# Performance work log

Measured on AMD Instinct MI355X. Metric: run time of the kernel, lower is better.

Reference implementation:

```python
import jax, jax.numpy as jnp
import numpy as np

EMBED_DIM = 128
NUM_SYMBOLS = 200000
PAD_IDX = NUM_SYMBOLS
PROCESS_STEPS = 4
LN_EPS = 1e-5
NEG_INF = -1.0e9


def _layernorm(x, g, b):
    m = jnp.mean(x, axis=-1, keepdims=True)
    v = jnp.var(x, axis=-1, keepdims=True)
    return (x - m) / jnp.sqrt(v + LN_EPS) * g + b


def setup_inputs() -> dict:
    key = jax.random.key(0)
    ks = jax.random.split(key, 32)
    d = EMBED_DIM
    B, FEW, K = 4096, 5, 50

    def n(i, shape, s=0.05):
        return jax.random.normal(ks[i], shape, dtype=jnp.float32) * s

    inp = {}
    inp["query"] = jax.random.randint(ks[0], (B, 2), 0, NUM_SYMBOLS)
    inp["support"] = jax.random.randint(ks[1], (FEW, 2), 0, NUM_SYMBOLS)
    inp["q_l1"] = jax.random.randint(ks[2], (B, K, 2), 0, NUM_SYMBOLS + 1)
    inp["q_deg_l"] = jax.random.randint(ks[3], (B,), 0, K + 1)
    inp["q_r1"] = jax.random.randint(ks[4], (B, K, 2), 0, NUM_SYMBOLS + 1)
    inp["q_deg_r"] = jax.random.randint(ks[5], (B,), 0, K + 1)
    inp["s_l1"] = jax.random.randint(ks[6], (FEW, K, 2), 0, NUM_SYMBOLS + 1)
    inp["s_deg_l"] = jax.random.randint(ks[7], (FEW,), 0, K + 1)
    inp["s_r1"] = jax.random.randint(ks[8], (FEW, K, 2), 0, NUM_SYMBOLS + 1)
    inp["s_deg_r"] = jax.random.randint(ks[9], (FEW,), 0, K + 1)
    # Embedding table with zeroed padding row (nn.Embedding padding_idx semantics)
    inp["emb"] = n(10, (NUM_SYMBOLS + 1, d), 0.1).at[PAD_IDX].set(0.0)
    inp["gcn_W"] = n(11, (d, 2 * d))
    inp["gcn_lin_b"] = jnp.zeros((d,), jnp.float32)
    inp["gcn_b"] = jnp.zeros((d,), jnp.float32)
    inp["gate_temp"] = jnp.float32(1.0)
    inp["cg_W1"] = n(12, (d // 2, d))
    inp["cg_b1"] = jnp.zeros((d // 2,), jnp.float32)
    inp["cg_ln_g"] = jnp.ones((d // 2,), jnp.float32)
    inp["cg_ln_b"] = jnp.zeros((d // 2,), jnp.float32)
    inp["cg_W2"] = n(13, (1, d // 2))
    inp["cg_b2"] = jnp.zeros((1,), jnp.float32)
    dm = 2 * d  # d_model
    inp["se_W1"] = n(14, (2 * dm, dm))
    inp["se_b1"] = jnp.zeros((2 * dm,), jnp.float32)
    inp["se_W2"] = n(15, (dm, 2 * dm))
    inp["se_b2"] = jnp.zeros((dm,), jnp.float32)
    inp["se_ln_g"] = jnp.ones((dm,), jnp.float32)
    inp["se_ln_b"] = jnp.zeros((dm,), jnp.float32)
    hid = 2 * dm  # LSTMCell hidden size
    inp["lstm_Wih"] = n(16, (4 * hid, dm))
    inp["lstm_Whh"] = n(17, (4 * hid, hid))
    inp["lstm_bih"] = jnp.zeros((4 * hid,), jnp.float32)
    inp["lstm_bhh"] = jnp.zeros((4 * hid,), jnp.float32)
    return inp


def reference(query, support, q_l1, q_deg_l, q_r1, q_deg_r, s_l1, s_deg_l, s_r1, s_deg_r,
              emb, gcn_W, gcn_lin_b, gcn_b, gate_temp,
              cg_W1, cg_b1, cg_ln_g, cg_ln_b, cg_W2, cg_b2,
              se_W1, se_b1, se_W2, se_b2, se_ln_g, se_ln_b,
              lstm_Wih, lstm_Whh, lstm_bih, lstm_bhh):

    def neigh(conns, deg, self_ids):
        rel, ent = conns[..., 0], conns[..., 1]
        self_e = emb[self_ids]                                      # [N, d]
        cat = jnp.concatenate([emb[rel], emb[ent]], axis=-1)        # [N, K, 2d]
        proj = jnp.einsum('nkc,dc->nkd', cat, gcn_W) + gcn_lin_b + gcn_b
        proj = jax.nn.leaky_relu(proj, 0.01)                        # dropout = eval no-op
        scores = jnp.einsum('nkd,nd->nk', proj, self_e)
        scores = jnp.where(rel == PAD_IDX, NEG_INF, scores)
        w = jax.nn.softmax(scores, axis=1)
        agg = jnp.einsum('nk,nkd->nd', w, proj)                     # [N, d]
        h = jax.nn.relu(_layernorm(agg @ cg_W1.T + cg_b1, cg_ln_g, cg_ln_b))
        logit = h @ cg_W2.T + cg_b2                                 # [N, 1]
        temp = jnp.clip(gate_temp, 0.1, 5.0)
        gate = jax.nn.sigmoid(logit / temp)
        gate = gate * (deg > 0).astype(jnp.float32)[:, None]
        return jnp.tanh(self_e + gate * agg)

    def support_enc(x):  # residual FFN + LayerNorm
        h = jax.nn.relu(x @ se_W1.T + se_b1)
        return _layernorm(h @ se_W2.T + se_b2 + x, se_ln_g, se_ln_b)

    q_vec = jnp.concatenate([neigh(q_l1, q_deg_l, query[:, 0]),
                             neigh(q_r1, q_deg_r, query[:, 1])], axis=-1)   # [B, 2d]
    s_vec = jnp.concatenate([neigh(s_l1, s_deg_l, support[:, 0]),
                             neigh(s_r1, s_deg_r, support[:, 1])], axis=-1)  # [FEW, 2d]

    support_g = jnp.mean(support_enc(s_vec), axis=0, keepdims=True)  # [1, 2d]
    query_enc = support_enc(q_vec)                                   # [B, 2d]

    B, dm = query_enc.shape
    hid = 2 * dm

    def step(carry, _):
        h_r, c = carry
        gates = query_enc @ lstm_Wih.T + lstm_bih + h_r @ lstm_Whh.T + lstm_bhh
        i, f, g, o = jnp.split(gates, 4, axis=-1)  # torch LSTMCell gate order
        c = jax.nn.sigmoid(f) * c + jax.nn.sigmoid(i) * jnp.tanh(g)
        h_cell = jax.nn.sigmoid(o) * jnp.tanh(c)
        h = query_enc + h_cell[:, :dm]
        attn = jax.nn.softmax(h @ support_g.T, axis=1)  # [B, 1]
        r = attn @ support_g
        return (jnp.concatenate([h, r], axis=1), c), h

    init = (jnp.zeros((B, hid), query_enc.dtype), jnp.zeros((B, hid), query_enc.dtype))
    _, hs = jax.lax.scan(step, init, None, length=PROCESS_STEPS)
    query_g = hs[-1]
    return jnp.sum(query_g * support_g, axis=1)  # [B]
```

## Files before the change

### kernel.cpp

```cpp
#include <hip/hip_runtime.h>
#include <hip/hip_bf16.h>
#include <cstdint>
#include <cstddef>

#define PAD_IDX 200000
#define KN 50
#define MROWS 200001

using frag8 = __attribute__((ext_vector_type(8))) short;
using f32x4 = __attribute__((ext_vector_type(4))) float;

__device__ __forceinline__ short f2bf_rn(float v) {
    __hip_bfloat16 h = __float2bfloat16(v);
    union { __hip_bfloat16 h; short s; } u; u.h = h; return u.s;
}
__device__ __forceinline__ float bf2f(short s) {
    union { uint32_t u; float f; } x; x.u = ((uint32_t)(uint16_t)s) << 16;
    return x.f;
}
__device__ __forceinline__ float sigm(float x) { return 1.f / (1.f + __expf(-x)); }

__device__ __forceinline__ int lstm_perm(int c) {
    int u = c >> 6, g = (c >> 4) & 3, v = c & 15;
    return (g << 9) + (u << 4) + v;
}

__global__ void k_prep(const float* __restrict__ se_W1, const float* __restrict__ se_W2,
                       const float* __restrict__ gcn_W, const float* __restrict__ lin_b,
                       const float* __restrict__ gb,
                       const float* __restrict__ Wih, const float* __restrict__ Whh,
                       short* __restrict__ sw1, short* __restrict__ sw2,
                       short* __restrict__ Bmat, float* __restrict__ bias256,
                       short* __restrict__ Bih, short* __restrict__ Bhh) {
    int b = blockIdx.x, t = threadIdx.x;
    if (b < 512) {
        int i = b * 256 + t;
        sw1[i] = f2bf_rn(se_W1[i]);
    } else if (b < 1024) {
        int i = (b - 512) * 256 + t;
        sw2[i] = f2bf_rn(se_W2[i]);
    } else if (b < 1152) {
        int i = (b - 1024) * 256 + t;
        int n = i >> 7, k = i & 127;
        float v = (n < 128) ? gcn_W[n * 256 + k] : gcn_W[(n - 128) * 256 + 128 + k];
        Bmat[i] = f2bf_rn(v);
        if (k == 0) bias256[n] = (n < 128) ? 0.f : (lin_b[n - 128] + gb[n - 128]);
    } else {
        int i = (b - 1152) * 256 + t;
        int c = i >> 9, k = i & 511;
        int n = lstm_perm(c);
        if (k < 256) Bih[c * 256 + k] = f2bf_rn(Wih[n * 256 + k]);
        else         Bhh[c * 256 + (k - 256)] = f2bf_rn(Whh[(size_t)n * 512 + (k - 256)]);
    }
}


__global__ __launch_bounds__(256, 2) void k_table(
    const float* __restrict__ emb, const short* __restrict__ Bmat,
    const float* __restrict__ bias256, short* __restrict__ T)
{
    __shared__ short Bs[128 * 136];
    const int t = threadIdx.x, lane = t & 63, w = t >> 6;
    const int n0 = blockIdx.x * 128;
    const int l15 = lane & 15, lk = lane >> 4;

#pragma unroll
    for (int i = 0; i < 8; ++i) {
        int c = i * 256 + t;
        int row = c >> 4, k8 = (c & 15) << 3;
        *reinterpret_cast<frag8*>(&Bs[row * 136 + k8]) =
            *reinterpret_cast<const frag8*>(Bmat + (n0 + row) * 128 + k8);
    }
    __syncthreads();

    frag8 bq[8][4];
#pragma unroll
    for (int fn = 0; fn < 8; ++fn)
#pragma unroll
        for (int kf = 0; kf < 4; ++kf)
            bq[fn][kf] = *reinterpret_cast<const frag8*>(
                &Bs[(fn * 16 + l15) * 136 + kf * 32 + (lk << 3)]);
    float bc[8];
#pragma unroll
    for (int fn = 0; fn < 8; ++fn) bc[fn] = bias256[n0 + fn * 16 + l15];
    __syncthreads();

    const int rbase = w * 32;
    for (int tile = blockIdx.y; tile < 1563; tile += gridDim.y) {
        const int m0 = tile * 128;
        f32x4 acc[2][8] = {};
#pragma unroll
        for (int kf = 0; kf < 4; ++kf) {
            frag8 af[2];
#pragma unroll
            for (int fm = 0; fm < 2; ++fm) {
                int row = m0 + rbase + fm * 16 + l15;
                frag8 av = {0, 0, 0, 0, 0, 0, 0, 0};
                if (row < MROWS) {
                    const float* p = emb + (size_t)row * 128 + kf * 32 + (lk << 3);
                    float4 v0 = *reinterpret_cast<const float4*>(p);
                    float4 v1 = *reinterpret_cast<const float4*>(p + 4);
                    av[0] = f2bf_rn(v0.x); av[1] = f2bf_rn(v0.y);
                    av[2] = f2bf_rn(v0.z); av[3] = f2bf_rn(v0.w);
                    av[4] = f2bf_rn(v1.x); av[5] = f2bf_rn(v1.y);
                    av[6] = f2bf_rn(v1.z); av[7] = f2bf_rn(v1.w);
                }
                af[fm] = av;
            }
#pragma unroll
            for (int fn = 0; fn < 8; ++fn) {
                acc[0][fn] = __builtin_amdgcn_mfma_f32_16x16x32_bf16(af[0], bq[fn][kf], acc[0][fn], 0, 0, 0);
                acc[1][fn] = __builtin_amdgcn_mfma_f32_16x16x32_bf16(af[1], bq[fn][kf], acc[1][fn], 0, 0, 0);
            }
        }
#pragma unroll
        for (int fm = 0; fm < 2; ++fm)
#pragma unroll
            for (int fn = 0; fn < 8; ++fn)
#pragma unroll
                for (int j = 0; j < 4; ++j) {
                    int lrow = rbase + fm * 16 + (lk << 2) + j;
                    Bs[lrow * 136 + fn * 16 + l15] = f2bf_rn(acc[fm][fn][j] + bc[fn]);
                }
#pragma unroll
        for (int p = 0; p < 8; ++p) {
            int idx = p * 64 + lane;
            int rl = idx >> 4, ch = idx & 15;
            int srow = rbase + rl;
            int grow = m0 + srow;
            if (grow < MROWS) {
                frag8 v = *reinterpret_cast<const frag8*>(&Bs[srow * 136 + ch * 8]);
                *reinterpret_cast<frag8*>(T + (size_t)grow * 256 + n0 + ch * 8) = v;
            }
        }
    }
}


constexpr int SA = 40;
constexpr int CS = 132;

template<bool RELU, bool OUTBF>
__global__ __launch_bounds__(256) void gemm_bt(
    const short* __restrict__ A, int lda, const short* __restrict__ B, int ldb,
    float* __restrict__ C, short* __restrict__ Cbf, int ldc,
    const float* __restrict__ bias, int M, int N, int K)
{
    __shared__ short sh[2 * 128 * SA];
    short* As = sh;
    short* Bs = sh + 128 * SA;
    const int t = threadIdx.x;
    const int m0 = blockIdx.y * 128, n0 = blockIdx.x * 128;
    const int wave = t >> 6, lane = t & 63;
    const int wr = wave >> 1, wc = wave & 1;
    f32x4 acc[4][4] = {};
    for (int k0 = 0; k0 < K; k0 += 32) {
#pragma unroll
        for (int i = 0; i < 2; ++i) {
            int idx = t + i * 256;
            int r = idx >> 2, c8 = (idx & 3) << 3;
            frag8 av = {0, 0, 0, 0, 0, 0, 0, 0};
            int arow = m0 + r;
            if (arow < M)
                av = *reinterpret_cast<const frag8*>(A + (size_t)arow * lda + k0 + c8);
            *reinterpret_cast<frag8*>(&As[r * SA + c8]) = av;
            frag8 bv = *reinterpret_cast<const frag8*>(B + (size_t)(n0 + r) * ldb + k0 + c8);
            *reinterpret_cast<frag8*>(&Bs[r * SA + c8]) = bv;
        }
        __syncthreads();
        frag8 af[4], bfv[4];
#pragma unroll
        for (int f = 0; f < 4; ++f) {
            af[f]  = *reinterpret_cast<const frag8*>(&As[(wr * 64 + f * 16 + (lane & 15)) * SA + ((lane >> 4) << 3)]);
            bfv[f] = *reinterpret_cast<const frag8*>(&Bs[(wc * 64 + f * 16 + (lane & 15)) * SA + ((lane >> 4) << 3)]);
        }
#pragma unroll
        for (int fm = 0; fm < 4; ++fm)
#pragma unroll
            for (int fn = 0; fn < 4; ++fn)
                acc[fm][fn] = __builtin_amdgcn_mfma_f32_16x16x32_bf16(af[fm], bfv[fn], acc[fm][fn], 0, 0, 0);
        __syncthreads();
    }

    if constexpr (OUTBF) {
#pragma unroll
        for (int half = 0; half < 2; ++half) {
            if (wr == half) {
#pragma unroll
                for (int fm = 0; fm < 4; ++fm) {
                    int rl = fm * 16 + ((lane >> 4) << 2);
#pragma unroll
                    for (int fn = 0; fn < 4; ++fn) {
                        int col = wc * 64 + fn * 16 + (lane & 15);
                        float bcv = bias[n0 + col];
#pragma unroll
                        for (int j = 0; j < 4; ++j) {
                            float v = acc[fm][fn][j] + bcv;
                            if (RELU) v = fmaxf(v, 0.f);
                            sh[(rl + j) * CS + col] = f2bf_rn(v);
                        }
                    }
                }
            }
            __syncthreads();
#pragma unroll
            for (int p = 0; p < 4; ++p) {
                int off16 = p * 256 + t;
                int rl = off16 >> 4, ch = off16 & 15;
                int rr = m0 + half * 64 + rl;
                if (rr < M) {
                    frag8 val = *reinterpret_cast<const frag8*>(&sh[rl * CS + ch * 8]);
                    *reinterpret_cast<frag8*>(&Cbf[(size_t)rr * ldc + n0 + ch * 8]) = val;
                }
            }
            __syncthreads();
        }
    } else {
#pragma unroll
        for (int fm = 0; fm < 4; ++fm) {
            int rowb = m0 + wr * 64 + fm * 16 + ((lane >> 4) << 2);
#pragma unroll
            for (int fn = 0; fn < 4; ++fn) {
                int col = n0 + wc * 64 + fn * 16 + (lane & 15);
                float bcv = bias[col];
#pragma unroll
                for (int j = 0; j < 4; ++j) {
                    int rr = rowb + j;
                    if (rr < M) {
                        float v = acc[fm][fn][j] + bcv;
                        if (RELU) v = fmaxf(v, 0.f);
                        C[(size_t)rr * ldc + col] = v;
                    }
                }
            }
        }
    }
}


__global__ __launch_bounds__(256) void gemm_lstm2(
    const short* __restrict__ A, const short* __restrict__ Bp,
    const float* __restrict__ G0, const float* __restrict__ whh_r,
    float* __restrict__ cbuf, const float* __restrict__ enc,
    float* __restrict__ hbuf, short* __restrict__ AHnext, int last)
{
    __shared__ short sh[2 * 128 * SA];
    short* As = sh;
    short* Bs = sh + 128 * SA;
    const int t = threadIdx.x;
    const int m0 = blockIdx.y * 128, n0 = blockIdx.x * 128;
    const int wave = t >> 6, lane = t & 63;
    const int wr = wave >> 1, wc = wave & 1;
    f32x4 acc[4][4] = {};
    for (int k0 = 0; k0 < 256; k0 += 32) {
#pragma unroll
        for (int i = 0; i < 2; ++i) {
            int idx = t + i * 256;
            int r = idx >> 2, c8 = (idx & 3) << 3;
            frag8 av = *reinterpret_cast<const frag8*>(A + (size_t)(m0 + r) * 512 + k0 + c8);
            *reinterpret_cast<frag8*>(&As[r * SA + c8]) = av;
            frag8 bv = *reinterpret_cast<const frag8*>(Bp + (size_t)(n0 + r) * 256 + k0 + c8);
            *reinterpret_cast<frag8*>(&Bs[r * SA + c8]) = bv;
        }
        __syncthreads();
        frag8 af[4], bfv[4];
#pragma unroll
        for (int f = 0; f < 4; ++f) {
            af[f]  = *reinterpret_cast<const frag8*>(&As[(wr * 64 + f * 16 + (lane & 15)) * SA + ((lane >> 4) << 3)]);
            bfv[f] = *reinterpret_cast<const frag8*>(&Bs[(wc * 64 + f * 16 + (lane & 15)) * SA + ((lane >> 4) << 3)]);
        }
#pragma unroll
        for (int fm = 0; fm < 4; ++fm)
#pragma unroll
            for (int fn = 0; fn < 4; ++fn)
                acc[fm][fn] = __builtin_amdgcn_mfma_f32_16x16x32_bf16(af[fm], bfv[fn], acc[fm][fn], 0, 0, 0);
        __syncthreads();
    }

    const int v = lane & 15;
    const int colbase = n0 + wc * 64;
    const int j = ((blockIdx.x * 2 + wc) << 4) + v;
    float wr0 = whh_r[colbase + v];
    float wr1 = whh_r[colbase + 16 + v];
    float wr2 = whh_r[colbase + 32 + v];
    float wr3 = whh_r[colbase + 48 + v];
#pragma unroll
    for (int fm = 0; fm < 4; ++fm) {
        int rowb = m0 + wr * 64 + fm * 16 + ((lane >> 4) << 2);
#pragma unroll
        for (int jr = 0; jr < 4; ++jr) {
            int row = rowb + jr;
            const float* g0p = G0 + (size_t)row * 2048 + colbase;
            float gi = acc[fm][0][jr] + g0p[v]      + wr0;
            float gf = acc[fm][1][jr] + g0p[16 + v] + wr1;
            float gg = acc[fm][2][jr] + g0p[32 + v] + wr2;
            float go = acc[fm][3][jr] + g0p[48 + v] + wr3;
            size_t cidx = (size_t)row * 512 + j;
            float cn = sigm(gf) * cbuf[cidx] + sigm(gi) * tanhf(gg);
            cbuf[cidx] = cn;
            float hc = sigm(go) * tanhf(cn);
            if (j < 256) {
                float hv = enc[(size_t)row * 256 + j] + hc;
                AHnext[(size_t)row * 512 + 256 + j] = f2bf_rn(hv);
                if (last) hbuf[(size_t)row * 256 + j] = hv;
            }
        }
    }
}


__global__ void k_lstm0(const float* __restrict__ G0, float* __restrict__ cbuf,
                        const float* __restrict__ enc, short* __restrict__ AHnext) {
    int idx = blockIdx.x * 256 + threadIdx.x;
    int row = idx >> 9, j = idx & 511;
    int u = j >> 4, v = j & 15;
    const float* gp = G0 + (size_t)row * 2048 + (u << 6);
    float gi = gp[v], gg = gp[32 + v], go = gp[48 + v];
    float cn = sigm(gi) * tanhf(gg);
    cbuf[idx] = cn;
    float hc = sigm(go) * tanhf(cn);
    if (j < 256) {
        float hv = enc[(size_t)row * 256 + j] + hc;
        AHnext[(size_t)row * 512 + 256 + j] = f2bf_rn(hv);
    }
}


constexpr int PS2 = 136;

__global__ __launch_bounds__(128) void k_neigh(
    const int* __restrict__ q_l1, const int* __restrict__ q_deg_l,
    const int* __restrict__ q_r1, const int* __restrict__ q_deg_r,
    const int* __restrict__ s_l1, const int* __restrict__ s_deg_l,
    const int* __restrict__ s_r1, const int* __restrict__ s_deg_r,
    const int* __restrict__ query, const int* __restrict__ support,
    const float* __restrict__ emb, const short* __restrict__ T,
    const float* __restrict__ cg_W1, const float* __restrict__ cg_b1,
    const float* __restrict__ cg_ln_g, const float* __restrict__ cg_ln_b,
    const float* __restrict__ cg_W2, const float* __restrict__ cg_b2,
    const float* __restrict__ temp_p,
    float* __restrict__ outv, short* __restrict__ outbf)
{
    int b = blockIdx.x;
    const int* conns; const int* deg; const int* ids2; int side, n, orow;
    if (b < 4096)      { conns = q_l1; deg = q_deg_l; ids2 = query;   side = 0; n = b;        orow = n; }
    else if (b < 8192) { conns = q_r1; deg = q_deg_r; ids2 = query;   side = 1; n = b - 4096; orow = n; }
    else if (b < 8197) { conns = s_l1; deg = s_deg_l; ids2 = support; side = 0; n = b - 8192; orow = 4096 + n; }
    else               { conns = s_r1; deg = s_deg_r; ids2 = support; side = 1; n = b - 8197; orow = 4096 + n; }

    int t = threadIdx.x;
    __shared__ __align__(16) short projb[KN * PS2];
    __shared__ __align__(16) float se[128];
    __shared__ int rels[KN], ents[KN];
    __shared__ float wts[KN];
    __shared__ float scs[KN];
    __shared__ __align__(16) float aggs[128];
    __shared__ float gate_s;

    int self_id = ids2[n * 2 + side];
    float self_e = emb[(size_t)self_id * 128 + t];
    se[t] = self_e;
    if (t < KN) {
        rels[t] = conns[((size_t)n * KN + t) * 2];
        ents[t] = conns[((size_t)n * KN + t) * 2 + 1];
    }
    __syncthreads();

#pragma unroll 10
    for (int k = 0; k < KN; ++k) {
        int r = rels[k], e = ents[k];
        float raw = bf2f(T[(size_t)r * 256 + t]) + bf2f(T[(size_t)e * 256 + 128 + t]);
        float p = raw > 0.f ? raw : 0.01f * raw;
        projb[k * PS2 + t] = f2bf_rn(p);
    }
    __syncthreads();

    {
        int k = t >> 1, hf = t & 1;
        float s = 0.f;
        if (k < KN) {
            const short* pr = &projb[k * PS2 + hf * 64];
            const float* seh = &se[hf * 64];
#pragma unroll
            for (int i = 0; i < 8; ++i) {
                frag8 v = *reinterpret_cast<const frag8*>(pr + i * 8);
#pragma unroll
                for (int q = 0; q < 8; ++q) s += bf2f(v[q]) * seh[i * 8 + q];
            }
            s += __shfl_xor(s, 1);
            if (hf == 0) scs[k] = (rels[k] == PAD_IDX) ? -1e9f : s;
        }
    }
    __syncthreads();

    if (t < 64) {
        float sc = (t < KN) ? scs[t] : -1e9f;
        float m = sc;
        for (int o = 32; o; o >>= 1) m = fmaxf(m, __shfl_xor(m, o));
        float e = (t < KN) ? __expf(sc - m) : 0.f;
        float ssum = e;
        for (int o = 32; o; o >>= 1) ssum += __shfl_xor(ssum, o);
        if (t < KN) wts[t] = e / ssum;
    }
    __syncthreads();

    float agg = 0.f;
#pragma unroll 10
    for (int k = 0; k < KN; ++k) agg += wts[k] * bf2f(projb[k * PS2 + t]);
    aggs[t] = agg;
    __syncthreads();

    if (t < 64) {
        const float4* w1 = reinterpret_cast<const float4*>(cg_W1 + t * 128);
        const float4* a4 = reinterpret_cast<const float4*>(aggs);
        float acc = cg_b1[t];
#pragma unroll 8
        for (int d = 0; d < 32; ++d) {
            float4 a = a4[d], ww = w1[d];
            acc += a.x * ww.x + a.y * ww.y + a.z * ww.z + a.w * ww.w;
        }
        float s = acc;
        for (int o = 32; o; o >>= 1) s += __shfl_xor(s, o);
        float mean = s * (1.f / 64.f);
        float dv = acc - mean;
        float vs = dv * dv;
        for (int o = 32; o; o >>= 1) vs += __shfl_xor(vs, o);
        float var = vs * (1.f / 64.f);
        float hv = dv * rsqrtf(var + 1e-5f) * cg_ln_g[t] + cg_ln_b[t];
        hv = fmaxf(hv, 0.f);
        float lg = hv * cg_W2[t];
        for (int o = 32; o; o >>= 1) lg += __shfl_xor(lg, o);
        if (t == 0) {
            lg += cg_b2[0];
            float temp = fminf(fmaxf(temp_p[0], 0.1f), 5.0f);
            float gate = sigm(lg / temp);
            gate_s = (deg[n] > 0) ? gate : 0.f;
        }
    }
    __syncthreads();

    float o = tanhf(self_e + gate_s * agg);
    size_t off = (size_t)orow * 256 + (size_t)side * 128 + t;
    outv[off] = o;
    outbf[off] = f2bf_rn(o);
}


__global__ void k_ln(const float* __restrict__ se2out, const float* __restrict__ x,
                     const float* __restrict__ g, const float* __restrict__ b,
                     float* __restrict__ enc, short* __restrict__ AHa,
                     short* __restrict__ AHb, int M) {
    int wave = threadIdx.x >> 6, lane = threadIdx.x & 63;
    int row = blockIdx.x * 4 + wave;
    if (row >= M) return;
    const float* pr = se2out + (size_t)row * 256;
    const float* px = x + (size_t)row * 256;
    float v[4];
    float s = 0.f;
#pragma unroll
    for (int i = 0; i < 4; ++i) { v[i] = pr[lane + 64 * i] + px[lane + 64 * i]; s += v[i]; }
    for (int o = 32; o; o >>= 1) s += __shfl_xor(s, o);
    float mean = s * (1.f / 256.f);
    float vs = 0.f;
#pragma unroll
    for (int i = 0; i < 4; ++i) { float d = v[i] - mean; vs += d * d; }
    for (int o = 32; o; o >>= 1) vs += __shfl_xor(vs, o);
    float inv = rsqrtf(vs * (1.f / 256.f) + 1e-5f);
#pragma unroll
    for (int i = 0; i < 4; ++i) {
        int col = lane + 64 * i;
        float ov = (v[i] - mean) * inv * g[col] + b[col];
        enc[(size_t)row * 256 + col] = ov;
        if (row < 4096) {
            short bf = f2bf_rn(ov);
            AHa[(size_t)row * 512 + col] = bf;
            AHb[(size_t)row * 512 + col] = bf;
        }
    }
}


__global__ void k_whhbias(const float* __restrict__ enc, const float* __restrict__ Whh,
                          const float* __restrict__ bih, const float* __restrict__ bhh,
                          float* __restrict__ sg, float* __restrict__ bias_a,
                          float* __restrict__ whh_r) {
    __shared__ __align__(16) float sgs[256];
    int t = threadIdx.x;
    float s0 = 0.f;
#pragma unroll
    for (int i = 0; i < 5; ++i) s0 += enc[(size_t)(4096 + i) * 256 + t];
    s0 *= 0.2f;
    sgs[t] = s0;
    if (blockIdx.x == 0) sg[t] = s0;
    __syncthreads();

    int c = blockIdx.x * 256 + t;
    int nn = lstm_perm(c);
    const float4* wr = reinterpret_cast<const float4*>(Whh + (size_t)nn * 512 + 256);
    const float4* g4 = reinterpret_cast<const float4*>(sgs);
    float s = 0.f;
#pragma unroll 8
    for (int q = 0; q < 64; ++q) {
        float4 a = g4[q], ww = wr[q];
        s += a.x * ww.x + a.y * ww.y + a.z * ww.z + a.w * ww.w;
    }
    bias_a[c] = bih[nn] + bhh[nn];
    whh_r[c] = s;
}

__global__ void k_dot(const float* __restrict__ h, const float* __restrict__ gvec,
                      float* __restrict__ out) {
    int wave = threadIdx.x >> 6, lane = threadIdx.x & 63;
    int n = blockIdx.x * 4 + wave;
    if (n >= 4096) return;
    const float* p = h + (size_t)n * 256;
    float s = 0.f;
#pragma unroll
    for (int i = 0; i < 4; ++i) s += p[lane + 64 * i] * gvec[lane + 64 * i];
    for (int o = 32; o; o >>= 1) s += __shfl_xor(s, o);
    if (!lane) out[n] = s;
}


extern "C" void kernel_launch(void* const* d_in, const int* in_sizes, int n_in,
                              void* d_out, int out_size, void* d_ws, size_t ws_size,
                              hipStream_t stream) {
    const int* query     = (const int*)d_in[0];
    const int* support   = (const int*)d_in[1];
    const int* q_l1      = (const int*)d_in[2];
    const int* q_deg_l   = (const int*)d_in[3];
    const int* q_r1      = (const int*)d_in[4];
    const int* q_deg_r   = (const int*)d_in[5];
    const int* s_l1      = (const int*)d_in[6];
    const int* s_deg_l   = (const int*)d_in[7];
    const int* s_r1      = (const int*)d_in[8];
    const int* s_deg_r   = (const int*)d_in[9];
    const float* emb     = (const float*)d_in[10];
    const float* gcn_W   = (const float*)d_in[11];
    const float* gcn_lin_b = (const float*)d_in[12];
    const float* gcn_b   = (const float*)d_in[13];
    const float* gate_temp = (const float*)d_in[14];
    const float* cg_W1   = (const float*)d_in[15];
    const float* cg_b1   = (const float*)d_in[16];
    const float* cg_ln_g = (const float*)d_in[17];
    const float* cg_ln_b = (const float*)d_in[18];
    const float* cg_W2   = (const float*)d_in[19];
    const float* cg_b2   = (const float*)d_in[20];
    const float* se_W1   = (const float*)d_in[21];
    const float* se_b1   = (const float*)d_in[22];
    const float* se_W2   = (const float*)d_in[23];
    const float* se_b2   = (const float*)d_in[24];
    const float* se_ln_g = (const float*)d_in[25];
    const float* se_ln_b = (const float*)d_in[26];
    const float* lstm_Wih = (const float*)d_in[27];
    const float* lstm_Whh = (const float*)d_in[28];
    const float* lstm_bih = (const float*)d_in[29];
    const float* lstm_bhh = (const float*)d_in[30];

    char* ws = (char*)d_ws;
    short* T       = (short*)(ws + 0);
    short* h1bf    = (short*)(ws + 0);
    float* se2out  = (float*)(ws + 4199424);
    float* enc     = (float*)(ws + 8398848);
    float* cbuf    = (float*)(ws + 12598272);
    float* hbuf    = (float*)(ws + 20986880);
    short* AHa     = (short*)(ws + 25181184);
    short* AHb     = (short*)(ws + 29375488);
    float* G0      = (float*)(ws + 33569792);
    float* qsvec   = (float*)(ws + 102400512);
    short* qsbf    = (short*)(ws + 106599936);
    short* Bmat    = (short*)(ws + 108699648);
    float* bias256 = (float*)(ws + 108765184);
    short* sw1     = (short*)(ws + 108766208);
    short* sw2     = (short*)(ws + 109028352);
    short* Bih     = (short*)(ws + 109290496);
    short* Bhh     = (short*)(ws + 110339072);
    float* sg      = (float*)(ws + 111387648);
    float* bias_a  = (float*)(ws + 111388672);
    float* whh_r   = (float*)(ws + 111396864);
    float* outp    = (float*)d_out;

    k_prep<<<5248, 256, 0, stream>>>(se_W1, se_W2, gcn_W, gcn_lin_b, gcn_b,
                                     lstm_Wih, lstm_Whh, sw1, sw2, Bmat, bias256, Bih, Bhh);

    k_table<<<dim3(2, 400), 256, 0, stream>>>(emb, Bmat, bias256, T);

    k_neigh<<<8202, 128, 0, stream>>>(q_l1, q_deg_l, q_r1, q_deg_r,
        s_l1, s_deg_l, s_r1, s_deg_r, query, support, emb, T,
        cg_W1, cg_b1, cg_ln_g, cg_ln_b, cg_W2, cg_b2, gate_temp, qsvec, qsbf);

    gemm_bt<true, true><<<dim3(4, 33), 256, 0, stream>>>(
        qsbf, 256, sw1, 256, nullptr, h1bf, 512, se_b1, 4101, 512, 256);
    gemm_bt<false, false><<<dim3(2, 33), 256, 0, stream>>>(
        h1bf, 512, sw2, 512, se2out, nullptr, 256, se_b2, 4101, 256, 512);
    k_ln<<<1026, 256, 0, stream>>>(se2out, qsvec, se_ln_g, se_ln_b, enc, AHa, AHb, 4101);

    k_whhbias<<<8, 256, 0, stream>>>(enc, lstm_Whh, lstm_bih, lstm_bhh, sg, bias_a, whh_r);

    gemm_bt<false, false><<<dim3(16, 32), 256, 0, stream>>>(
        AHa, 512, Bih, 256, G0, nullptr, 2048, bias_a, 4096, 2048, 256);

    k_lstm0<<<8192, 256, 0, stream>>>(G0, cbuf, enc, AHb);

    gemm_lstm2<<<dim3(16, 32), 256, 0, stream>>>(
        AHb + 256, Bhh, G0, whh_r, cbuf, enc, hbuf, AHa, 0);
    gemm_lstm2<<<dim3(16, 32), 256, 0, stream>>>(
        AHa + 256, Bhh, G0, whh_r, cbuf, enc, hbuf, AHb, 0);
    gemm_lstm2<<<dim3(16, 32), 256, 0, stream>>>(
        AHb + 256, Bhh, G0, whh_r, cbuf, enc, hbuf, AHa, 1);

    k_dot<<<1024, 256, 0, stream>>>(hbuf, sg, outp);
}
```

Before: 269.7 us.

## Pipeline embedding-table GEMM and fuse the first LSTM gate GEMM with step zero

```diff
diff --git a/kernel.cpp b/kernel.cpp
--- a/kernel.cpp
+++ b/kernel.cpp
@@ -55,84 +55,89 @@
 }
 
 
-__global__ __launch_bounds__(256, 2) void k_table(
+#define NT_TAB 3126
+
+__global__ __launch_bounds__(256) void k_table(
     const float* __restrict__ emb, const short* __restrict__ Bmat,
     const float* __restrict__ bias256, short* __restrict__ T)
 {
-    __shared__ short Bs[128 * 136];
+    __shared__ short Bs2[32 * 64 * 8];
+    __shared__ short bounce[64 * 136];
     const int t = threadIdx.x, lane = t & 63, w = t >> 6;
     const int n0 = blockIdx.x * 128;
     const int l15 = lane & 15, lk = lane >> 4;
+    const int rbase = w * 16;
 
 #pragma unroll
     for (int i = 0; i < 8; ++i) {
-        int c = i * 256 + t;
-        int row = c >> 4, k8 = (c & 15) << 3;
-        *reinterpret_cast<frag8*>(&Bs[row * 136 + k8]) =
-            *reinterpret_cast<const frag8*>(Bmat + (n0 + row) * 128 + k8);
-    }
-    __syncthreads();
-
-    frag8 bq[8][4];
-#pragma unroll
-    for (int fn = 0; fn < 8; ++fn)
-#pragma unroll
-        for (int kf = 0; kf < 4; ++kf)
-            bq[fn][kf] = *reinterpret_cast<const frag8*>(
-                &Bs[(fn * 16 + l15) * 136 + kf * 32 + (lk << 3)]);
+        int slot = i * 256 + t;
+        int fk = slot >> 6, ln = slot & 63;
+        int fn = fk >> 2, kf = fk & 3;
+        frag8 bv = *reinterpret_cast<const frag8*>(
+            Bmat + (n0 + fn * 16 + (ln & 15)) * 128 + kf * 32 + ((ln >> 4) << 3));
+        *reinterpret_cast<frag8*>(&Bs2[slot * 8]) = bv;
+    }
     float bc[8];
 #pragma unroll
     for (int fn = 0; fn < 8; ++fn) bc[fn] = bias256[n0 + fn * 16 + l15];
     __syncthreads();
 
-    const int rbase = w * 32;
-    for (int tile = blockIdx.y; tile < 1563; tile += gridDim.y) {
-        const int m0 = tile * 128;
-        f32x4 acc[2][8] = {};
+    auto issue = [&](int m0, float4* pv) {
+        int row = m0 + rbase + l15;
+        const float* p = emb + (size_t)row * 128 + (lk << 3);
+        bool ok = row < MROWS;
+        float4 z = {0.f, 0.f, 0.f, 0.f};
 #pragma unroll
         for (int kf = 0; kf < 4; ++kf) {
-            frag8 af[2];
-#pragma unroll
-            for (int fm = 0; fm < 2; ++fm) {
-                int row = m0 + rbase + fm * 16 + l15;
-                frag8 av = {0, 0, 0, 0, 0, 0, 0, 0};
-                if (row < MROWS) {
-                    const float* p = emb + (size_t)row * 128 + kf * 32 + (lk << 3);
-                    float4 v0 = *reinterpret_cast<const float4*>(p);
-                    float4 v1 = *reinterpret_cast<const float4*>(p + 4);
-                    av[0] = f2bf_rn(v0.x); av[1] = f2bf_rn(v0.y);
-                    av[2] = f2bf_rn(v0.z); av[3] = f2bf_rn(v0.w);
-                    av[4] = f2bf_rn(v1.x); av[5] = f2bf_rn(v1.y);
-                    av[6] = f2bf_rn(v1.z); av[7] = f2bf_rn(v1.w);
-                }
-                af[fm] = av;
-            }
+            pv[kf * 2]     = ok ? *reinterpret_cast<const float4*>(p + kf * 32)     : z;
+            pv[kf * 2 + 1] = ok ? *reinterpret_cast<const float4*>(p + kf * 32 + 4) : z;
+        }
+    };
+
+    auto compute_store = [&](int m0, const float4* pv) {
+        f32x4 acc[8] = {};
+#pragma unroll
+        for (int kf = 0; kf < 4; ++kf) {
+            float4 v0 = pv[kf * 2], v1 = pv[kf * 2 + 1];
+            frag8 av;
+            av[0] = f2bf_rn(v0.x); av[1] = f2bf_rn(v0.y);
+            av[2] = f2bf_rn(v0.z); av[3] = f2bf_rn(v0.w);
+            av[4] = f2bf_rn(v1.x); av[5] = f2bf_rn(v1.y);
+            av[6] = f2bf_rn(v1.z); av[7] = f2bf_rn(v1.w);
 #pragma unroll
             for (int fn = 0; fn < 8; ++fn) {
-                acc[0][fn] = __builtin_amdgcn_mfma_f32_16x16x32_bf16(af[0], bq[fn][kf], acc[0][fn], 0, 0, 0);
-                acc[1][fn] = __builtin_amdgcn_mfma_f32_16x16x32_bf16(af[1], bq[fn][kf], acc[1][fn], 0, 0, 0);
-            }
-        }
-#pragma unroll
-        for (int fm = 0; fm < 2; ++fm)
-#pragma unroll
-            for (int fn = 0; fn < 8; ++fn)
-#pragma unroll
-                for (int j = 0; j < 4; ++j) {
-                    int lrow = rbase + fm * 16 + (lk << 2) + j;
-                    Bs[lrow * 136 + fn * 16 + l15] = f2bf_rn(acc[fm][fn][j] + bc[fn]);
-                }
-#pragma unroll
-        for (int p = 0; p < 8; ++p) {
+                frag8 bf = *reinterpret_cast<const frag8*>(&Bs2[((fn * 4 + kf) * 64 + lane) * 8]);
+                acc[fn] = __builtin_amdgcn_mfma_f32_16x16x32_bf16(av, bf, acc[fn], 0, 0, 0);
+            }
+        }
+#pragma unroll
+        for (int fn = 0; fn < 8; ++fn)
+#pragma unroll
+            for (int j = 0; j < 4; ++j)
+                bounce[(rbase + (lk << 2) + j) * 136 + fn * 16 + l15] = f2bf_rn(acc[fn][j] + bc[fn]);
+#pragma unroll
+        for (int p = 0; p < 4; ++p) {
             int idx = p * 64 + lane;
             int rl = idx >> 4, ch = idx & 15;
-            int srow = rbase + rl;
-            int grow = m0 + srow;
+            int grow = m0 + rbase + rl;
             if (grow < MROWS) {
-                frag8 v = *reinterpret_cast<const frag8*>(&Bs[srow * 136 + ch * 8]);
+                frag8 v = *reinterpret_cast<const frag8*>(&bounce[(rbase + rl) * 136 + ch * 8]);
                 *reinterpret_cast<frag8*>(T + (size_t)grow * 256 + n0 + ch * 8) = v;
             }
         }
+    };
+
+    float4 pvA[8], pvB[8];
+    int tile = blockIdx.y;
+    const int stride = gridDim.y;
+    if (tile < NT_TAB) issue(tile * 64, pvA);
+    for (; tile < NT_TAB; tile += 2 * stride) {
+        int t1 = tile + stride;
+        if (t1 < NT_TAB) issue(t1 * 64, pvB);
+        compute_store(tile * 64, pvA);
+        int t2 = tile + 2 * stride;
+        if (t2 < NT_TAB) issue(t2 * 64, pvA);
+        if (t1 < NT_TAB) compute_store(t1 * 64, pvB);
     }
 }
 
@@ -238,9 +243,81 @@
 }
 
 
+__global__ __launch_bounds__(256) void gemm_g0(
+    const short* __restrict__ A, const short* __restrict__ Bih,
+    const float* __restrict__ bias_a, float* __restrict__ cbuf,
+    const float* __restrict__ enc, short* __restrict__ AHnext,
+    short* __restrict__ G0b)
+{
+    __shared__ short sh[2 * 128 * SA];
+    short* As = sh;
+    short* Bs = sh + 128 * SA;
+    const int t = threadIdx.x;
+    const int m0 = blockIdx.y * 128, n0 = blockIdx.x * 128;
+    const int wave = t >> 6, lane = t & 63;
+    const int wr = wave >> 1, wc = wave & 1;
+    f32x4 acc[4][4] = {};
+    for (int k0 = 0; k0 < 256; k0 += 32) {
+#pragma unroll
+        for (int i = 0; i < 2; ++i) {
+            int idx = t + i * 256;
+            int r = idx >> 2, c8 = (idx & 3) << 3;
+            frag8 av = *reinterpret_cast<const frag8*>(A + (size_t)(m0 + r) * 512 + k0 + c8);
+            *reinterpret_cast<frag8*>(&As[r * SA + c8]) = av;
+            frag8 bv = *reinterpret_cast<const frag8*>(Bih + (size_t)(n0 + r) * 256 + k0 + c8);
+            *reinterpret_cast<frag8*>(&Bs[r * SA + c8]) = bv;
+        }
+        __syncthreads();
+        frag8 af[4], bfv[4];
+#pragma unroll
+        for (int f = 0; f < 4; ++f) {
+            af[f]  = *reinterpret_cast<const frag8*>(&As[(wr * 64 + f * 16 + (lane & 15)) * SA + ((lane >> 4) << 3)]);
+            bfv[f] = *reinterpret_cast<const frag8*>(&Bs[(wc * 64 + f * 16 + (lane & 15)) * SA + ((lane >> 4) << 3)]);
+        }
+#pragma unroll
+        for (int fm = 0; fm < 4; ++fm)
+#pragma unroll
+            for (int fn = 0; fn < 4; ++fn)
+                acc[fm][fn] = __builtin_amdgcn_mfma_f32_16x16x32_bf16(af[fm], bfv[fn], acc[fm][fn], 0, 0, 0);
+        __syncthreads();
+    }
+
+    const int v = lane & 15;
+    const int colbase = n0 + wc * 64;
+    const int j = ((blockIdx.x * 2 + wc) << 4) + v;
+    float bv0 = bias_a[colbase + v];
+    float bv1 = bias_a[colbase + 16 + v];
+    float bv2 = bias_a[colbase + 32 + v];
+    float bv3 = bias_a[colbase + 48 + v];
+#pragma unroll
+    for (int fm = 0; fm < 4; ++fm) {
+        int rowb = m0 + wr * 64 + fm * 16 + ((lane >> 4) << 2);
+#pragma unroll
+        for (int jr = 0; jr < 4; ++jr) {
+            int row = rowb + jr;
+            float gi = acc[fm][0][jr] + bv0;
+            float gf = acc[fm][1][jr] + bv1;
+            float gg = acc[fm][2][jr] + bv2;
+            float go = acc[fm][3][jr] + bv3;
+            short4 g4;
+            g4.x = f2bf_rn(gi); g4.y = f2bf_rn(gf);
+            g4.z = f2bf_rn(gg); g4.w = f2bf_rn(go);
+            *reinterpret_cast<short4*>(G0b + ((size_t)row * 512 + j) * 4) = g4;
+            float cn = sigm(gi) * tanhf(gg);
+            cbuf[(size_t)row * 512 + j] = cn;
+            float hc = sigm(go) * tanhf(cn);
+            if (j < 256) {
+                float hv = enc[(size_t)row * 256 + j] + hc;
+                AHnext[(size_t)row * 512 + 256 + j] = f2bf_rn(hv);
+            }
+        }
+    }
+}
+
+
 __global__ __launch_bounds__(256) void gemm_lstm2(
     const short* __restrict__ A, const short* __restrict__ Bp,
-    const float* __restrict__ G0, const float* __restrict__ whh_r,
+    const short* __restrict__ G0b, const float* __restrict__ whh_r,
     float* __restrict__ cbuf, const float* __restrict__ enc,
     float* __restrict__ hbuf, short* __restrict__ AHnext, int last)
 {
@@ -290,11 +367,11 @@
 #pragma unroll
         for (int jr = 0; jr < 4; ++jr) {
             int row = rowb + jr;
-            const float* g0p = G0 + (size_t)row * 2048 + colbase;
-            float gi = acc[fm][0][jr] + g0p[v]      + wr0;
-            float gf = acc[fm][1][jr] + g0p[16 + v] + wr1;
-            float gg = acc[fm][2][jr] + g0p[32 + v] + wr2;
-            float go = acc[fm][3][jr] + g0p[48 + v] + wr3;
+            short4 g4 = *reinterpret_cast<const short4*>(G0b + ((size_t)row * 512 + j) * 4);
+            float gi = acc[fm][0][jr] + bf2f(g4.x) + wr0;
+            float gf = acc[fm][1][jr] + bf2f(g4.y) + wr1;
+            float gg = acc[fm][2][jr] + bf2f(g4.z) + wr2;
+            float go = acc[fm][3][jr] + bf2f(g4.w) + wr3;
             size_t cidx = (size_t)row * 512 + j;
             float cn = sigm(gf) * cbuf[cidx] + sigm(gi) * tanhf(gg);
             cbuf[cidx] = cn;
@@ -305,23 +382,6 @@
                 if (last) hbuf[(size_t)row * 256 + j] = hv;
             }
         }
-    }
-}
-
-
-__global__ void k_lstm0(const float* __restrict__ G0, float* __restrict__ cbuf,
-                        const float* __restrict__ enc, short* __restrict__ AHnext) {
-    int idx = blockIdx.x * 256 + threadIdx.x;
-    int row = idx >> 9, j = idx & 511;
-    int u = j >> 4, v = j & 15;
-    const float* gp = G0 + (size_t)row * 2048 + (u << 6);
-    float gi = gp[v], gg = gp[32 + v], go = gp[48 + v];
-    float cn = sigm(gi) * tanhf(gg);
-    cbuf[idx] = cn;
-    float hc = sigm(go) * tanhf(cn);
-    if (j < 256) {
-        float hv = enc[(size_t)row * 256 + j] + hc;
-        AHnext[(size_t)row * 512 + 256 + j] = f2bf_rn(hv);
     }
 }
 
@@ -448,8 +508,7 @@
 
 __global__ void k_ln(const float* __restrict__ se2out, const float* __restrict__ x,
                      const float* __restrict__ g, const float* __restrict__ b,
-                     float* __restrict__ enc, short* __restrict__ AHa,
-                     short* __restrict__ AHb, int M) {
+                     float* __restrict__ enc, short* __restrict__ AHa, int M) {
     int wave = threadIdx.x >> 6, lane = threadIdx.x & 63;
     int row = blockIdx.x * 4 + wave;
     if (row >= M) return;
@@ -471,11 +530,7 @@
         int col = lane + 64 * i;
         float ov = (v[i] - mean) * inv * g[col] + b[col];
         enc[(size_t)row * 256 + col] = ov;
-        if (row < 4096) {
-            short bf = f2bf_rn(ov);
-            AHa[(size_t)row * 512 + col] = bf;
-            AHb[(size_t)row * 512 + col] = bf;
-        }
+        if (row < 4096) AHa[(size_t)row * 512 + col] = f2bf_rn(ov);
     }
 }
 
@@ -566,7 +621,7 @@
     float* hbuf    = (float*)(ws + 20986880);
     short* AHa     = (short*)(ws + 25181184);
     short* AHb     = (short*)(ws + 29375488);
-    float* G0      = (float*)(ws + 33569792);
+    short* G0b     = (short*)(ws + 33569792);
     float* qsvec   = (float*)(ws + 102400512);
     short* qsbf    = (short*)(ws + 106599936);
     short* Bmat    = (short*)(ws + 108699648);
@@ -583,7 +638,7 @@
     k_prep<<<5248, 256, 0, stream>>>(se_W1, se_W2, gcn_W, gcn_lin_b, gcn_b,
                                      lstm_Wih, lstm_Whh, sw1, sw2, Bmat, bias256, Bih, Bhh);
 
-    k_table<<<dim3(2, 400), 256, 0, stream>>>(emb, Bmat, bias256, T);
+    k_table<<<dim3(2, 782), 256, 0, stream>>>(emb, Bmat, bias256, T);
 
     k_neigh<<<8202, 128, 0, stream>>>(q_l1, q_deg_l, q_r1, q_deg_r,
         s_l1, s_deg_l, s_r1, s_deg_r, query, support, emb, T,
@@ -593,21 +648,18 @@
         qsbf, 256, sw1, 256, nullptr, h1bf, 512, se_b1, 4101, 512, 256);
     gemm_bt<false, false><<<dim3(2, 33), 256, 0, stream>>>(
         h1bf, 512, sw2, 512, se2out, nullptr, 256, se_b2, 4101, 256, 512);
-    k_ln<<<1026, 256, 0, stream>>>(se2out, qsvec, se_ln_g, se_ln_b, enc, AHa, AHb, 4101);
+    k_ln<<<1026, 256, 0, stream>>>(se2out, qsvec, se_ln_g, se_ln_b, enc, AHa, 4101);
 
     k_whhbias<<<8, 256, 0, stream>>>(enc, lstm_Whh, lstm_bih, lstm_bhh, sg, bias_a, whh_r);
 
-    gemm_bt<false, false><<<dim3(16, 32), 256, 0, stream>>>(
-        AHa, 512, Bih, 256, G0, nullptr, 2048, bias_a, 4096, 2048, 256);
-
-    k_lstm0<<<8192, 256, 0, stream>>>(G0, cbuf, enc, AHb);
+    gemm_g0<<<dim3(16, 32), 256, 0, stream>>>(AHa, Bih, bias_a, cbuf, enc, AHb, G0b);
 
     gemm_lstm2<<<dim3(16, 32), 256, 0, stream>>>(
-        AHb + 256, Bhh, G0, whh_r, cbuf, enc, hbuf, AHa, 0);
+        AHb + 256, Bhh, G0b, whh_r, cbuf, enc, hbuf, AHa, 0);
     gemm_lstm2<<<dim3(16, 32), 256, 0, stream>>>(
-        AHa + 256, Bhh, G0, whh_r, cbuf, enc, hbuf, AHb, 0);
+        AHa + 256, Bhh, G0b, whh_r, cbuf, enc, hbuf, AHb, 0);
     gemm_lstm2<<<dim3(16, 32), 256, 0, stream>>>(
-        AHb + 256, Bhh, G0, whh_r, cbuf, enc, hbuf, AHa, 1);
+        AHb + 256, Bhh, G0b, whh_r, cbuf, enc, hbuf, AHa, 1);
 
     k_dot<<<1024, 256, 0, stream>>>(hbuf, sg, outp);
 }
```

New measurement: 319.0 us. 18.3% more time.
